# Kernel tuning notes

Measured on AMD Instinct MI355X. Metric: run time of the kernel, lower is better.

Reference implementation:

```python
import jax, jax.numpy as jnp
import numpy as np

HEADS = 8
DIM = 32  # dim_heads


def setup_inputs() -> dict:
    key = jax.random.key(0)
    k1, k2, k3, k4 = jax.random.split(key, 4)
    b, c, h, w = 8, 256, 128, 128
    hidden = HEADS * DIM  # 256
    x = jax.random.normal(k1, (b, c, h, w), dtype=jnp.float32)
    w_qkv = jax.random.normal(k2, (3 * hidden, c), dtype=jnp.float32) * 0.05
    w_out = jax.random.normal(k3, (c, hidden), dtype=jnp.float32) * 0.05
    b_out = jax.random.normal(k4, (c,), dtype=jnp.float32) * 0.05
    return {"x": x, "w_qkv": w_qkv, "w_out": w_out, "b_out": b_out}


def reference(x, w_qkv, w_out, b_out):
    b, c, h, w = x.shape
    n = h * w
    # 1x1 conv == channel matmul: [b, 3*heads*dim, h, w]
    qkv = jnp.einsum('bchw,oc->bohw', x, w_qkv)
    # rearrange 'b (qkv heads c) h w -> qkv b heads c (h w)'
    qkv = qkv.reshape(b, 3, HEADS, DIM, n)
    q, k, v = qkv[:, 0], qkv[:, 1], qkv[:, 2]  # each [b, heads, dim, n]
    k = jax.nn.softmax(k, axis=-1)
    # context: [b, heads, dim, dim]
    context = jnp.einsum('bhdn,bhen->bhde', k, v)
    o = jnp.einsum('bhde,bhdn->bhen', context, q)  # [b, heads, dim, n]
    o = o.reshape(b, HEADS * DIM, h, w)
    # out 1x1 conv with bias
    o = jnp.einsum('bchw,oc->bohw', o, w_out) + b_out[None, :, None, None]
    return o
```

## Files before the change

### kernel.cpp

```cpp
#include <hip/hip_runtime.h>
#include <hip/hip_bf16.h>
#include <cstdint>

#define NPIX 16384
#define BATCH 8
#define CDIM 256

typedef __bf16 bh8 __attribute__((ext_vector_type(8)));
typedef __bf16 bh4 __attribute__((ext_vector_type(4)));
typedef float  fx4 __attribute__((ext_vector_type(4)));

__device__ __forceinline__ void gload16(const void* g, void* l) {
  __builtin_amdgcn_global_load_lds(
      (const __attribute__((address_space(1))) uint32_t*)g,
      (__attribute__((address_space(3))) uint32_t*)l, 16, 0, 0);
}

__device__ __forceinline__ fx4 mfma16(bh8 a, bh8 b, fx4 c) {
  return __builtin_amdgcn_mfma_f32_16x16x32_bf16(a, b, c, 0, 0, 0);
}

__device__ __forceinline__ void pbar() {
  asm volatile("" ::: "memory");
  __builtin_amdgcn_s_barrier();
  asm volatile("" ::: "memory");
}
#define VMWI(n) asm volatile("s_waitcnt vmcnt(" #n ")" ::: "memory")

__global__ __launch_bounds__(256) void prep_w(const float* __restrict__ w_qkv,
                                              __bf16* __restrict__ wqb,
                                              __bf16* __restrict__ wqT) {
  __shared__ float tile[32][33];
  int bid = blockIdx.x;
  if (bid < 512) {
    int i = bid * 256 + threadIdx.x;
    wqb[i] = (__bf16)w_qkv[256 * 256 + i];
  } else {
    bid -= 512;
    const int t0 = (bid & 7) * 32, o0 = (bid >> 3) * 32;
    const int tx = threadIdx.x & 31, ty = threadIdx.x >> 5;
#pragma unroll
    for (int j = 0; j < 4; ++j) {
      int r = ty * 4 + j;
      tile[r][tx] = w_qkv[(size_t)(o0 + r) * 256 + t0 + tx];
    }
    __syncthreads();
#pragma unroll
    for (int j = 0; j < 4; ++j) {
      int tl = ty * 4 + j;
      wqT[(size_t)(t0 + tl) * 256 + o0 + tx] = (__bf16)tile[tx][tl];
    }
  }
}

__global__ __launch_bounds__(256) void transpose_x(const float* __restrict__ x,
                                                   __bf16* __restrict__ xT) {
  __shared__ float tf[64][68];
  const int n0 = blockIdx.x * 64, c0 = blockIdx.y * 64, b = blockIdx.z;
  const int u = threadIdx.x;
#pragma unroll
  for (int i = 0; i < 4; ++i) {
    int j = i * 256 + u;
    int r = j >> 4, q = j & 15;
    *(fx4*)&tf[r][q * 4] =
        *(const fx4*)&x[((size_t)b * CDIM + c0 + r) * NPIX + n0 + q * 4];
  }
  __syncthreads();
  const int nl = u >> 2, cq = (u & 3) * 16;
#pragma unroll
  for (int w = 0; w < 2; ++w) {
    bh8 v;
#pragma unroll
    for (int j = 0; j < 8; ++j) v[j] = (__bf16)tf[cq + w * 8 + j][nl];
    *(bh8*)&xT[((size_t)b * NPIX + n0 + nl) * CDIM + c0 + cq + w * 8] = v;
  }
}


#define BSP ((__bf16*)(smem + 16384))

#define STA(kt)                                                                \
  do {                                                                         \
    _Pragma("unroll") for (int i_ = 0; i_ < 4; ++i_) {                         \
      int j_ = i_ * 256 + tid;                                                 \
      int row_ = j_ >> 3, c_ = j_ & 7;                                         \
      int sc_ = c_ ^ (row_ & 7);                                               \
      const __bf16* sb_;                                                       \
      if (EPI == 0) sb_ = (i_ < 2) ? Abk + (size_t)row_ * 256                  \
                                   : Abv + (size_t)(row_ - 64) * 256;          \
      else          sb_ = Ab + (size_t)row_ * 256;                             \
      gload16(sb_ + (kt)*64 + sc_ * 8, (__bf16*)smem + j_ * 8);                \
    }                                                                          \
  } while (0)

#define STB(kt)                                                                \
  do {                                                                         \
    _Pragma("unroll") for (int i_ = 0; i_ < 4; ++i_) {                         \
      int j_ = i_ * 256 + tid;                                                 \
      int row_ = j_ >> 3, c_ = j_ & 7;                                         \
      int sc_ = c_ ^ (row_ & 7);                                               \
      gload16(Bb + (size_t)row_ * 256 + (kt)*64 + sc_ * 8, BSP + j_ * 8);      \
    }                                                                          \
  } while (0)

#define COMP()                                                                 \
  do {                                                                         \
    _Pragma("unroll") for (int ks_ = 0; ks_ < 2; ++ks_) {                      \
      bh8 a_[4], b_[4];                                                        \
      const int swk_ = (ks_ * 4 + fq) ^ (fr & 7);                              \
      _Pragma("unroll") for (int m_ = 0; m_ < 4; ++m_)                         \
        a_[m_] = *(const bh8*)&((__bf16*)smem)[(wm * 64 + m_ * 16 + fr) * 64 + \
                                               swk_ * 8];                      \
      _Pragma("unroll") for (int n_ = 0; n_ < 4; ++n_)                         \
        b_[n_] = *(const bh8*)&BSP[(wn * 64 + n_ * 16 + fr) * 64 + swk_ * 8];  \
      _Pragma("unroll") for (int m_ = 0; m_ < 4; ++m_)                         \
      _Pragma("unroll") for (int n_ = 0; n_ < 4; ++n_)                         \
        acc[m_][n_] = mfma16(a_[m_], b_[n_], acc[m_][n_]);                     \
    }                                                                          \
  } while (0)

template <int EPI>
__global__ __launch_bounds__(256, 4) void gemm256(
    const __bf16* __restrict__ A, const __bf16* __restrict__ Bx,
    float* __restrict__ S_part, float* __restrict__ Zpart,
    const float* __restrict__ bias, float* __restrict__ fout) {
  __shared__ __align__(16) char smem[33024];
  const int tid = threadIdx.x;
  const int by = blockIdx.x;
  const int bx = blockIdx.y;
  const int b = blockIdx.z;
  const int lane = tid & 63, wid = tid >> 6;
  const int wm = wid >> 1, wn = wid & 1;
  const int fr = lane & 15, fq = lane >> 4;
  const int hp = by;
  const __bf16* Abk = A + (size_t)(hp * 64) * 256;
  const __bf16* Abv = A + (size_t)(256 + hp * 64) * 256;
  const __bf16* Ab  = A + (size_t)b * 65536 + (size_t)by * 128 * 256;
  const __bf16* Bb = Bx + ((size_t)b * NPIX + (size_t)bx * 128) * 256;

  fx4 acc[4][4] = {};

  STA(0); STB(0); VMWI(0); pbar(); COMP(); pbar();
  STA(1); STB(1); VMWI(0); pbar(); COMP(); pbar();
  STA(2); STB(2); VMWI(0); pbar(); COMP(); pbar();
  STA(3); STB(3); VMWI(0); pbar(); COMP(); pbar();

  if (EPI == 0) {
    float* zrow = (float*)(smem + 32768);
    if (tid < 64) zrow[tid] = 0.f;
#pragma unroll
    for (int m = 0; m < 4; ++m)
#pragma unroll
      for (int n = 0; n < 4; ++n)
#pragma unroll
        for (int j = 0; j < 4; ++j) {
          int r = m * 16 + fq * 4 + j;
          int px = wn * 64 + n * 16 + fr;
          int pc = px >> 3;
          int byo = r * 256 + ((pc ^ (r & 7)) << 4) + (px & 7) * 2;
          if (wm == 0)
            *(__bf16*)(smem + byo) = (__bf16)__expf(acc[m][n][j]);
          else
            *(__bf16*)(smem + 16384 + byo) = (__bf16)acc[m][n][j];
        }
    pbar();
    {
      int r = tid >> 2, c0 = (tid & 3) * 32;
      float za = 0.f;
#pragma unroll
      for (int i2 = 0; i2 < 4; ++i2) {
        int pc = (c0 + i2 * 8) >> 3;
        bh8 ev = *(const bh8*)(smem + r * 256 + ((pc ^ (r & 7)) << 4));
#pragma unroll
        for (int jj = 0; jj < 8; ++jj) za += (float)ev[jj];
      }
      atomicAdd(&zrow[r], za);
    }
    fx4 sac0 = {}, sac1 = {};
#pragma unroll
    for (int t2 = 0; t2 < 2; ++t2) {
      int tk = wid * 2 + t2;
      int hl = tk >> 2, quad = tk & 3;
      int drow = (quad >> 1) * 16, erow = (quad & 1) * 16;
      fx4 sac = {};
#pragma unroll
      for (int kt2 = 0; kt2 < 4; ++kt2) {
        int ra = hl * 32 + drow + fr;
        int rb = hl * 32 + erow + fr;
        int pc = kt2 * 4 + fq;
        bh8 af = *(const bh8*)(smem + ra * 256 + ((pc ^ (ra & 7)) << 4));
        bh8 bf = *(const bh8*)(smem + 16384 + rb * 256 + ((pc ^ (rb & 7)) << 4));
        sac = mfma16(af, bf, sac);
      }
      if (t2 == 0) sac0 = sac; else sac1 = sac;
    }
    pbar();
    float* Sb = (float*)smem;
#pragma unroll
    for (int t2 = 0; t2 < 2; ++t2) {
      int tk = wid * 2 + t2;
      int hl = tk >> 2, quad = tk & 3;
      int drow = (quad >> 1) * 16, erow = (quad & 1) * 16;
      fx4 sv = (t2 == 0) ? sac0 : sac1;
#pragma unroll
      for (int j = 0; j < 4; ++j)
        Sb[hl * 1024 + (drow + fq * 4 + j) * 32 + erow + fr] = sv[j];
    }
    __syncthreads();
    {
      int hl = tid >> 7, idx = tid & 127;
      float* sp = S_part + ((size_t)((b * 8 + hp * 2 + hl) * 128 + bx)) * 1024;
      fx4 v0 = *(const fx4*)&Sb[hl * 1024 + idx * 8];
      fx4 v1 = *(const fx4*)&Sb[hl * 1024 + idx * 8 + 4];
      *(fx4*)&sp[idx * 8] = v0;
      *(fx4*)&sp[idx * 8 + 4] = v1;
    }
    if (tid < 64) {
      int head = hp * 2 + (tid >> 5);
      Zpart[((size_t)(b * 8 + head) * 128 + bx) * 32 + (tid & 31)] = zrow[tid];
    }
  } else {
    const size_t obase =
        (size_t)b * CDIM * NPIX + (size_t)(by * 128) * NPIX + (size_t)bx * 128;
    float* Ls = (float*)smem;
#pragma unroll
    for (int m = 0; m < 4; ++m) {
      __syncthreads();
#pragma unroll
      for (int n = 0; n < 4; ++n)
#pragma unroll
        for (int j = 0; j < 4; ++j)
          Ls[(wm * 16 + fq * 4 + j) * 132 + wn * 64 + n * 16 + fr] =
              acc[m][n][j] + bias[by * 128 + wm * 64 + m * 16 + fq * 4 + j];
      __syncthreads();
#pragma unroll
      for (int it = 0; it < 4; ++it) {
        int u = it * 256 + tid;
        int rr = u >> 5, cc = u & 31;
        int gch = (rr >> 4) * 64 + m * 16 + (rr & 15);
        fx4 val = *(const fx4*)&Ls[rr * 132 + cc * 4];
        *(fx4*)&fout[obase + (size_t)gch * NPIX + cc * 4] = val;
      }
    }
  }
}

__global__ __launch_bounds__(256) void reduce_w2(const float* __restrict__ S_part,
                                                 const float* __restrict__ Zpart,
                                                 const float* __restrict__ w_out,
                                                 __bf16* __restrict__ W2b) {
  const int seg = blockIdx.x;
  const int bh = blockIdx.y;
  const int b = bh >> 3, h = bh & 7;
  const int t = threadIdx.x;
  __shared__ float zs[8];
  __shared__ float ctxl[256];
  if (t < 8) zs[t] = 0.f;
  __syncthreads();
  {
    int row = seg * 8 + (t >> 5);
    float z = 0.f;
    for (int ch = (t & 31); ch < 128; ch += 32)
      z += Zpart[((size_t)bh * 128 + ch) * 32 + row];
    atomicAdd(&zs[t >> 5], z);
  }
  __syncthreads();
  const int i = seg * 256 + t;
  float s = 0.f;
  for (int ch = 0; ch < 128; ++ch) s += S_part[((size_t)bh * 128 + ch) * 1024 + i];
  ctxl[t] = s / zs[t >> 5];
  __syncthreads();
  const float* wrow = w_out + t * 256 + h * 32;
  float wv[32];
#pragma unroll
  for (int e = 0; e < 32; ++e) wv[e] = wrow[e];
#pragma unroll
  for (int dp = 0; dp < 8; ++dp) {
    float sacc = 0.f;
#pragma unroll
    for (int e = 0; e < 32; ++e) sacc += wv[e] * ctxl[dp * 32 + e];
    W2b[((size_t)b * 256 + t) * 256 + h * 32 + seg * 8 + dp] = (__bf16)sacc;
  }
}

__global__ __launch_bounds__(256) void make_w3(const __bf16* __restrict__ W2b,
                                               const __bf16* __restrict__ wqT,
                                               __bf16* __restrict__ W3) {
  const int bx = blockIdx.x, by = blockIdx.y, b = blockIdx.z;
  const int lane = threadIdx.x & 63, wid = threadIdx.x >> 6;
  const int wm = wid >> 1, wn = wid & 1;
  const int fr = lane & 15, fq = lane >> 4;
  const __bf16* Ab = W2b + (size_t)b * 65536 + (size_t)(by * 128 + wm * 64) * 256;
  const __bf16* Bb = wqT + (size_t)(bx * 128 + wn * 64) * 256;
  fx4 acc[4][4] = {};
#pragma unroll
  for (int h = 0; h < 8; ++h) {
    bh8 a_[4], b_[4];
#pragma unroll
    for (int m = 0; m < 4; ++m)
      a_[m] = *(const bh8*)(Ab + (size_t)(m * 16 + fr) * 256 + h * 32 + fq * 8);
#pragma unroll
    for (int n = 0; n < 4; ++n)
      b_[n] = *(const bh8*)(Bb + (size_t)(n * 16 + fr) * 256 + h * 32 + fq * 8);
#pragma unroll
    for (int m = 0; m < 4; ++m)
#pragma unroll
      for (int n = 0; n < 4; ++n) acc[m][n] = mfma16(a_[m], b_[n], acc[m][n]);
  }
#pragma unroll
  for (int m = 0; m < 4; ++m)
#pragma unroll
    for (int n = 0; n < 4; ++n) {
      int r0 = by * 128 + wm * 64 + m * 16 + fq * 4;
      int t0 = bx * 128 + wn * 64 + n * 16 + fr;
#pragma unroll
      for (int j = 0; j < 4; ++j)
        W3[(size_t)b * 65536 + (size_t)(r0 + j) * 256 + t0] = (__bf16)acc[m][n][j];
    }
}

extern "C" void kernel_launch(void* const* d_in, const int* in_sizes, int n_in,
                              void* d_out, int out_size, void* d_ws, size_t ws_size,
                              hipStream_t stream) {
  const float* x     = (const float*)d_in[0];
  const float* w_qkv = (const float*)d_in[1];
  const float* w_out = (const float*)d_in[2];
  const float* b_out = (const float*)d_in[3];
  float* out = (float*)d_out;

  char* ws = (char*)d_ws;
  __bf16* xT    = (__bf16*)(ws);
  __bf16* wqb   = (__bf16*)(ws + 67108864ull);
  __bf16* wqT   = (__bf16*)(ws + 67371008ull);
  __bf16* W2b   = (__bf16*)(ws + 67502080ull);
  __bf16* W3    = (__bf16*)(ws + 68550656ull);
  float*  S_part= (float*) (ws + 69599232ull);
  float*  Zpart = (float*) (ws + 103153664ull);

  prep_w<<<576, 256, 0, stream>>>(w_qkv, wqb, wqT);
  transpose_x<<<dim3(NPIX / 64, CDIM / 64, BATCH), 256, 0, stream>>>(x, xT);
  gemm256<0><<<dim3(4, NPIX / 128, BATCH), 256, 0, stream>>>(
      wqb, xT, S_part, Zpart, nullptr, nullptr);
  reduce_w2<<<dim3(4, 64), 256, 0, stream>>>(S_part, Zpart, w_out, W2b);
  make_w3<<<dim3(2, 2, BATCH), 256, 0, stream>>>(W2b, wqT, W3);
  gemm256<1><<<dim3(2, NPIX / 128, BATCH), 256, 0, stream>>>(
      W3, xT, nullptr, nullptr, b_out, out);
}
```

Baseline: 171.6 us.

## Fuse x transpose and bf16 cast into GEMM B-tile staging

```diff
diff --git a/kernel.cpp b/kernel.cpp
--- a/kernel.cpp
+++ b/kernel.cpp
@@ -25,7 +25,6 @@
   __builtin_amdgcn_s_barrier();
   asm volatile("" ::: "memory");
 }
-#define VMWI(n) asm volatile("s_waitcnt vmcnt(" #n ")" ::: "memory")
 
 __global__ __launch_bounds__(256) void prep_w(const float* __restrict__ w_qkv,
                                               __bf16* __restrict__ wqb,
@@ -53,31 +52,6 @@
   }
 }
 
-__global__ __launch_bounds__(256) void transpose_x(const float* __restrict__ x,
-                                                   __bf16* __restrict__ xT) {
-  __shared__ float tf[64][68];
-  const int n0 = blockIdx.x * 64, c0 = blockIdx.y * 64, b = blockIdx.z;
-  const int u = threadIdx.x;
-#pragma unroll
-  for (int i = 0; i < 4; ++i) {
-    int j = i * 256 + u;
-    int r = j >> 4, q = j & 15;
-    *(fx4*)&tf[r][q * 4] =
-        *(const fx4*)&x[((size_t)b * CDIM + c0 + r) * NPIX + n0 + q * 4];
-  }
-  __syncthreads();
-  const int nl = u >> 2, cq = (u & 3) * 16;
-#pragma unroll
-  for (int w = 0; w < 2; ++w) {
-    bh8 v;
-#pragma unroll
-    for (int j = 0; j < 8; ++j) v[j] = (__bf16)tf[cq + w * 8 + j][nl];
-    *(bh8*)&xT[((size_t)b * NPIX + n0 + nl) * CDIM + c0 + cq + w * 8] = v;
-  }
-}
-
-
-#define BSP ((__bf16*)(smem + 16384))
 
 #define STA(kt)                                                                \
   do {                                                                         \
@@ -93,15 +67,26 @@
     }                                                                          \
   } while (0)
 
-#define STB(kt)                                                                \
+#define BSTG(kt, rr2)                                                          \
   do {                                                                         \
-    _Pragma("unroll") for (int i_ = 0; i_ < 4; ++i_) {                         \
-      int j_ = i_ * 256 + tid;                                                 \
-      int row_ = j_ >> 3, c_ = j_ & 7;                                         \
-      int sc_ = c_ ^ (row_ & 7);                                               \
-      gload16(Bb + (size_t)row_ * 256 + (kt)*64 + sc_ * 8, BSP + j_ * 8);      \
+    const float* xr_ = Xb + (size_t)((kt)*64 + (rr2)*32 + cq * 4) * NPIX +     \
+                       pxb * 4;                                                \
+    fx4 r0_ = *(const fx4*)(xr_);                                              \
+    fx4 r1_ = *(const fx4*)(xr_ + NPIX);                                       \
+    fx4 r2_ = *(const fx4*)(xr_ + 2 * NPIX);                                   \
+    fx4 r3_ = *(const fx4*)(xr_ + 3 * NPIX);                                   \
+    const int chunk_ = (rr2)*4 + (cq >> 1);                                    \
+    _Pragma("unroll") for (int j_ = 0; j_ < 4; ++j_) {                         \
+      int px_ = pxb * 4 + j_;                                                  \
+      int byo_ = px_ * 128 + ((chunk_ ^ (px_ & 7)) << 4) + (cq & 1) * 8;       \
+      bh4 pk_;                                                                 \
+      pk_[0] = (__bf16)r0_[j_]; pk_[1] = (__bf16)r1_[j_];                      \
+      pk_[2] = (__bf16)r2_[j_]; pk_[3] = (__bf16)r3_[j_];                      \
+      *(bh4*)(smem + 16384 + byo_) = pk_;                                      \
     }                                                                          \
   } while (0)
+
+#define BSP ((__bf16*)(smem + 16384))
 
 #define COMP()                                                                 \
   do {                                                                         \
@@ -120,8 +105,8 @@
   } while (0)
 
 template <int EPI>
-__global__ __launch_bounds__(256, 4) void gemm256(
-    const __bf16* __restrict__ A, const __bf16* __restrict__ Bx,
+__global__ __launch_bounds__(256, 3) void gemm256(
+    const __bf16* __restrict__ A, const float* __restrict__ X,
     float* __restrict__ S_part, float* __restrict__ Zpart,
     const float* __restrict__ bias, float* __restrict__ fout) {
   __shared__ __align__(16) char smem[33024];
@@ -132,18 +117,19 @@
   const int lane = tid & 63, wid = tid >> 6;
   const int wm = wid >> 1, wn = wid & 1;
   const int fr = lane & 15, fq = lane >> 4;
+  const int cq = tid & 7, pxb = tid >> 3;
   const int hp = by;
   const __bf16* Abk = A + (size_t)(hp * 64) * 256;
   const __bf16* Abv = A + (size_t)(256 + hp * 64) * 256;
   const __bf16* Ab  = A + (size_t)b * 65536 + (size_t)by * 128 * 256;
-  const __bf16* Bb = Bx + ((size_t)b * NPIX + (size_t)bx * 128) * 256;
+  const float* Xb = X + (size_t)b * CDIM * NPIX + (size_t)bx * 128;
 
   fx4 acc[4][4] = {};
 
-  STA(0); STB(0); VMWI(0); pbar(); COMP(); pbar();
-  STA(1); STB(1); VMWI(0); pbar(); COMP(); pbar();
-  STA(2); STB(2); VMWI(0); pbar(); COMP(); pbar();
-  STA(3); STB(3); VMWI(0); pbar(); COMP(); pbar();
+  STA(0); BSTG(0, 0); BSTG(0, 1); __syncthreads(); COMP(); pbar();
+  STA(1); BSTG(1, 0); BSTG(1, 1); __syncthreads(); COMP(); pbar();
+  STA(2); BSTG(2, 0); BSTG(2, 1); __syncthreads(); COMP(); pbar();
+  STA(3); BSTG(3, 0); BSTG(3, 1); __syncthreads(); COMP(); pbar();
 
   if (EPI == 0) {
     float* zrow = (float*)(smem + 32768);
@@ -329,20 +315,18 @@
   float* out = (float*)d_out;
 
   char* ws = (char*)d_ws;
-  __bf16* xT    = (__bf16*)(ws);
-  __bf16* wqb   = (__bf16*)(ws + 67108864ull);
-  __bf16* wqT   = (__bf16*)(ws + 67371008ull);
-  __bf16* W2b   = (__bf16*)(ws + 67502080ull);
-  __bf16* W3    = (__bf16*)(ws + 68550656ull);
-  float*  S_part= (float*) (ws + 69599232ull);
-  float*  Zpart = (float*) (ws + 103153664ull);
+  __bf16* wqb   = (__bf16*)(ws);
+  __bf16* wqT   = (__bf16*)(ws + 262144ull);
+  __bf16* W2b   = (__bf16*)(ws + 393216ull);
+  __bf16* W3    = (__bf16*)(ws + 1441792ull);
+  float*  S_part= (float*) (ws + 2490368ull);
+  float*  Zpart = (float*) (ws + 36044800ull);
 
   prep_w<<<576, 256, 0, stream>>>(w_qkv, wqb, wqT);
-  transpose_x<<<dim3(NPIX / 64, CDIM / 64, BATCH), 256, 0, stream>>>(x, xT);
   gemm256<0><<<dim3(4, NPIX / 128, BATCH), 256, 0, stream>>>(
-      wqb, xT, S_part, Zpart, nullptr, nullptr);
+      wqb, x, S_part, Zpart, nullptr, nullptr);
   reduce_w2<<<dim3(4, 64), 256, 0, stream>>>(S_part, Zpart, w_out, W2b);
   make_w3<<<dim3(2, 2, BATCH), 256, 0, stream>>>(W2b, wqT, W3);
   gemm256<1><<<dim3(2, NPIX / 128, BATCH), 256, 0, stream>>>(
-      W3, xT, nullptr, nullptr, b_out, out);
-}
+      W3, x, nullptr, nullptr, b_out, out);
+}
```

After: 187.2 us. 9.1% more time.
